# Performance work log

Hardware: AMD Instinct MI355X
Metric: run time of the kernel (lower is better)

The kernel has to match this reference:

```python
import jax, jax.numpy as jnp
import numpy as np

B, N = 2, 2000
C_IN, RH, RW = 256, 7, 7
D_FLAT = C_IN * RH * RW  # 12544
D_OUT = 1024
NUM_CLASSES = 10


def setup_inputs() -> dict:
    key = jax.random.key(0)
    ks = jax.random.split(key, 10)
    s1 = 1.0 / np.sqrt(D_FLAT)
    s2 = 1.0 / np.sqrt(D_OUT)
    return {
        "features": jax.random.normal(ks[0], (B, N, C_IN, RH, RW), jnp.float32),
        "boxes": jax.random.normal(ks[1], (B, N, 5), jnp.float32),
        "w1": jax.random.uniform(ks[2], (D_FLAT, D_OUT), jnp.float32, -s1, s1),
        "b1": jax.random.uniform(ks[3], (D_OUT,), jnp.float32, -s1, s1),
        "w2": jax.random.uniform(ks[4], (D_OUT, D_OUT), jnp.float32, -s2, s2),
        "b2": jax.random.uniform(ks[5], (D_OUT,), jnp.float32, -s2, s2),
        "wc": jax.random.uniform(ks[6], (D_OUT, NUM_CLASSES + 1), jnp.float32, -s2, s2),
        "bc": jax.random.uniform(ks[7], (NUM_CLASSES + 1,), jnp.float32, -s2, s2),
        "wr": jax.random.uniform(ks[8], (D_OUT, 5), jnp.float32, -s2, s2),
        "br": jax.random.uniform(ks[9], (5,), jnp.float32, -s2, s2),
    }


def reference(features, boxes, w1, b1, w2, b2, wc, bc, wr, br):
    # Flatten(start_dim=2): [B, N, C*7*7]
    x = features.reshape(B, N, D_FLAT)
    # fc: Linear -> ReLU -> Linear -> ReLU
    h = jax.nn.relu(jnp.einsum("bnd,de->bne", x, w1) + b1)
    h = jax.nn.relu(jnp.einsum("bnd,de->bne", h, w2) + b2)
    classification = jnp.einsum("bnd,dc->bnc", h, wc) + bc  # [B, N, num_classes+1]
    regression = jnp.einsum("bnd,dr->bnr", h, wr) + br      # [B, N, 5]
    boxes_out = boxes + regression
    rois = boxes
    return classification, boxes_out, rois
```

## Files before the change

kernel.cpp:

```cpp
#include <hip/hip_runtime.h>
#include <stdint.h>

#define GAS __attribute__((address_space(1)))
#define LAS __attribute__((address_space(3)))

typedef short bf16x8 __attribute__((ext_vector_type(8)));
typedef float f32x4 __attribute__((ext_vector_type(4)));
typedef unsigned short u16x8 __attribute__((ext_vector_type(8)));

__device__ __forceinline__ unsigned short f2bf(float f) {
  union { float f; uint32_t u; } v; v.f = f;
  uint32_t r = v.u + 0x7FFFu + ((v.u >> 16) & 1u);
  return (unsigned short)(r >> 16);
}

__global__ __launch_bounds__(256) void prep_transpose(const float* __restrict__ w1,
                                                      const float* __restrict__ w2,
                                                      unsigned short* __restrict__ W1T,
                                                      unsigned short* __restrict__ W2T) {
  __shared__ unsigned short tile[32][33];
  int tx = threadIdx.x, ty = threadIdx.y;
  const float* src;
  unsigned short* dst;
  int R, yb;
  if ((int)blockIdx.y < 392) {
    src = w1; dst = W1T; R = 12544; yb = blockIdx.y;
  } else {
    src = w2; dst = W2T; R = 1024; yb = blockIdx.y - 392;
  }
  const int C = 1024;
  int r0 = yb * 32, c0 = blockIdx.x * 32;
#pragma unroll
  for (int i = 0; i < 32; i += 8)
    tile[ty + i][tx] = f2bf(src[(long)(r0 + ty + i) * C + c0 + tx]);
  __syncthreads();
#pragma unroll
  for (int i = 0; i < 32; i += 8)
    dst[(long)(c0 + ty + i) * R + r0 + tx] = tile[tx][ty + i];
}

__global__ __launch_bounds__(256, 2) void gemm1_f32a(const float* __restrict__ A,
                                                     const unsigned short* __restrict__ Bt,
                                                     float* __restrict__ Cv, int M, int K,
                                                     int kIters) {
  __shared__ unsigned short lA[128 * 64];
  __shared__ unsigned short lB[128 * 64];
  const int tid = threadIdx.x;
  const int lane = tid & 63;
  const int wave = tid >> 6;
  const int wm = wave >> 1, wn = wave & 1;

  const int b = blockIdx.x;
  const int xcd = b & 7;
  const int slot = b >> 3;
  const int bx = slot & 7;
  const int pg = xcd * 16 + (slot >> 3);
  const int by = pg & 31;
  const int bz = pg >> 5;

  const long rowBase = (long)by * 128;
  const long colBase = (long)bx * 128;
  const int kStart = bz * kIters * 64;

  f32x4 acc[4][4];
#pragma unroll
  for (int i = 0; i < 4; i++)
#pragma unroll
    for (int j = 0; j < 4; j++) acc[i][j] = (f32x4){0.f, 0.f, 0.f, 0.f};

  long gA[4], gB[4];
  int aLds[4];
#pragma unroll
  for (int it = 0; it < 4; ++it) {
    int f = it * 256 + tid;
    int r = f >> 3;
    int q = f & 7;
    int kq = ((q ^ (r & 7)) * 8) + kStart;
    long ar = rowBase + r;
    if (ar >= M) ar = M - 1;
    gA[it] = ar * (long)K + kq;
    gB[it] = ((long)(colBase + r)) * K + kq;
    aLds[it] = f * 8;
  }

  for (int ki = 0; ki < kIters; ++ki) {
    const long kc = (long)ki * 64;
#pragma unroll
    for (int it = 0; it < 4; ++it) {
      int f = it * 256 + tid;
      __builtin_amdgcn_global_load_lds((const GAS void*)(Bt + gB[it] + kc),
                                       (LAS void*)(lB + f * 8), 16, 0, 0);
    }
#pragma unroll
    for (int it = 0; it < 4; ++it) {
      const float4* p = (const float4*)(A + gA[it] + kc);
      float4 a = p[0], c = p[1];
      u16x8 v;
      v[0] = f2bf(a.x); v[1] = f2bf(a.y); v[2] = f2bf(a.z); v[3] = f2bf(a.w);
      v[4] = f2bf(c.x); v[5] = f2bf(c.y); v[6] = f2bf(c.z); v[7] = f2bf(c.w);
      *(u16x8*)(lA + aLds[it]) = v;
    }
    __syncthreads();
#pragma unroll
    for (int ks = 0; ks < 64; ks += 32) {
      bf16x8 af[4], bf[4];
      const int c = (ks >> 3) + (lane >> 4);
      const int slotk = (c ^ (lane & 7)) << 3;
      const int mr = wm * 64 + (lane & 15);
      const int nr = wn * 64 + (lane & 15);
#pragma unroll
      for (int i = 0; i < 4; i++)
        af[i] = *(const bf16x8*)(lA + (mr + i * 16) * 64 + slotk);
#pragma unroll
      for (int i = 0; i < 4; i++)
        bf[i] = *(const bf16x8*)(lB + (nr + i * 16) * 64 + slotk);
#pragma unroll
      for (int i = 0; i < 4; i++)
#pragma unroll
        for (int j = 0; j < 4; j++)
          acc[i][j] = __builtin_amdgcn_mfma_f32_16x16x32_bf16(af[i], bf[j], acc[i][j], 0, 0, 0);
    }
    __syncthreads();
  }

  const int cq = lane & 15;
  const int rq = (lane >> 4) * 4;
#pragma unroll
  for (int i = 0; i < 4; i++) {
#pragma unroll
    for (int j = 0; j < 4; j++) {
      int col = (int)colBase + wn * 64 + j * 16 + cq;
#pragma unroll
      for (int r = 0; r < 4; r++) {
        long grow = rowBase + wm * 64 + i * 16 + rq + r;
        if (grow < M) unsafeAtomicAdd(&Cv[grow * 1024 + col], acc[i][j][r]);
      }
    }
  }
}

__global__ __launch_bounds__(256, 2) void gemm2_fused(const float* __restrict__ H1f,
                                                      const float* __restrict__ bias1,
                                                      const unsigned short* __restrict__ Bt,
                                                      const float* __restrict__ bias2,
                                                      float* __restrict__ Cv, int M) {
  const int K = 1024;
  __shared__ unsigned short lA[128 * 64];
  __shared__ unsigned short lB[64 * 64];
  const int tid = threadIdx.x;
  const int lane = tid & 63;
  const int wave = tid >> 6;
  const int wm = wave >> 1, wn = wave & 1;

  const int b = blockIdx.x;
  const int xcd = b & 7;
  const int slot = b >> 3;
  const int bx = slot & 15;
  const int by = xcd * 4 + (slot >> 4);

  const long rowBase = (long)by * 128;
  const long colBase = (long)bx * 64;

  f32x4 acc[4][2];
#pragma unroll
  for (int i = 0; i < 4; i++)
#pragma unroll
    for (int j = 0; j < 2; j++) acc[i][j] = (f32x4){0.f, 0.f, 0.f, 0.f};

  long gA[4];
  int aLds[4], aKq[4];
#pragma unroll
  for (int it = 0; it < 4; ++it) {
    int f = it * 256 + tid;
    int r = f >> 3;
    int q = f & 7;
    int kq = (q ^ (r & 7)) * 8;
    long ar = rowBase + r;
    if (ar >= M) ar = M - 1;
    gA[it] = ar * (long)K + kq;
    aLds[it] = f * 8;
    aKq[it] = kq;
  }
  long gB[2];
#pragma unroll
  for (int it = 0; it < 2; ++it) {
    int f = it * 256 + tid;
    int r = f >> 3;
    int q = f & 7;
    int kq = (q ^ (r & 7)) * 8;
    gB[it] = ((long)(colBase + r)) * K + kq;
  }

  for (int ki = 0; ki < 16; ++ki) {
    const long kc = (long)ki * 64;
#pragma unroll
    for (int it = 0; it < 2; ++it) {
      int f = it * 256 + tid;
      __builtin_amdgcn_global_load_lds((const GAS void*)(Bt + gB[it] + kc),
                                       (LAS void*)(lB + f * 8), 16, 0, 0);
    }
#pragma unroll
    for (int it = 0; it < 4; ++it) {
      const float4* p = (const float4*)(H1f + gA[it] + kc);
      const float4* bp = (const float4*)(bias1 + kc + aKq[it]);
      float4 a = p[0], c = p[1];
      float4 ba = bp[0], bb = bp[1];
      u16x8 v;
      v[0] = f2bf(fmaxf(a.x + ba.x, 0.f)); v[1] = f2bf(fmaxf(a.y + ba.y, 0.f));
      v[2] = f2bf(fmaxf(a.z + ba.z, 0.f)); v[3] = f2bf(fmaxf(a.w + ba.w, 0.f));
      v[4] = f2bf(fmaxf(c.x + bb.x, 0.f)); v[5] = f2bf(fmaxf(c.y + bb.y, 0.f));
      v[6] = f2bf(fmaxf(c.z + bb.z, 0.f)); v[7] = f2bf(fmaxf(c.w + bb.w, 0.f));
      *(u16x8*)(lA + aLds[it]) = v;
    }
    __syncthreads();
#pragma unroll
    for (int ks = 0; ks < 64; ks += 32) {
      bf16x8 af[4], bf[2];
      const int c = (ks >> 3) + (lane >> 4);
      const int slotk = (c ^ (lane & 7)) << 3;
      const int mr = wm * 64 + (lane & 15);
      const int nr = wn * 32 + (lane & 15);
#pragma unroll
      for (int i = 0; i < 4; i++)
        af[i] = *(const bf16x8*)(lA + (mr + i * 16) * 64 + slotk);
#pragma unroll
      for (int j = 0; j < 2; j++)
        bf[j] = *(const bf16x8*)(lB + (nr + j * 16) * 64 + slotk);
#pragma unroll
      for (int i = 0; i < 4; i++)
#pragma unroll
        for (int j = 0; j < 2; j++)
          acc[i][j] = __builtin_amdgcn_mfma_f32_16x16x32_bf16(af[i], bf[j], acc[i][j], 0, 0, 0);
    }
    __syncthreads();
  }

  const int cq = lane & 15;
  const int rq = (lane >> 4) * 4;
#pragma unroll
  for (int i = 0; i < 4; i++) {
#pragma unroll
    for (int j = 0; j < 2; j++) {
      int col = (int)colBase + wn * 32 + j * 16 + cq;
      float bv = bias2[col];
#pragma unroll
      for (int r = 0; r < 4; r++) {
        long grow = rowBase + wm * 64 + i * 16 + rq + r;
        if (grow < M) {
          float v = acc[i][j][r] + bv;
          Cv[grow * 1024 + col] = v > 0.f ? v : 0.f;
        }
      }
    }
  }
}

__global__ __launch_bounds__(256) void head_kernel(
    const float* __restrict__ H2, const float* __restrict__ wc, const float* __restrict__ bc,
    const float* __restrict__ wr, const float* __restrict__ br, const float* __restrict__ boxes,
    float* __restrict__ cls, float* __restrict__ bout, float* __restrict__ rois) {
  const int lane = threadIdx.x & 63;
  const int wave = threadIdx.x >> 6;
  const int row = blockIdx.x * 4 + wave;
  const float* h = H2 + (long)row * 1024;
  float acc[16];
#pragma unroll
  for (int c = 0; c < 16; c++) acc[c] = 0.f;
#pragma unroll
  for (int i = 0; i < 16; i++) {
    int d = i * 64 + lane;
    float hv = h[d];
#pragma unroll
    for (int c = 0; c < 11; c++) acc[c] += hv * wc[d * 11 + c];
#pragma unroll
    for (int c = 0; c < 5; c++) acc[11 + c] += hv * wr[d * 5 + c];
  }
#pragma unroll
  for (int off = 32; off >= 1; off >>= 1) {
#pragma unroll
    for (int c = 0; c < 16; c++) acc[c] += __shfl_down(acc[c], off);
  }
  if (lane == 0) {
#pragma unroll
    for (int c = 0; c < 11; c++) cls[row * 11 + c] = acc[c] + bc[c];
#pragma unroll
    for (int c = 0; c < 5; c++) {
      float rg = acc[11 + c] + br[c];
      float bx = boxes[row * 5 + c];
      bout[row * 5 + c] = bx + rg;
      rois[row * 5 + c] = bx;
    }
  }
}

extern "C" void kernel_launch(void* const* d_in, const int* in_sizes, int n_in,
                              void* d_out, int out_size, void* d_ws, size_t ws_size,
                              hipStream_t stream) {
  const float* features = (const float*)d_in[0];
  const float* boxes = (const float*)d_in[1];
  const float* w1 = (const float*)d_in[2];
  const float* b1 = (const float*)d_in[3];
  const float* w2 = (const float*)d_in[4];
  const float* b2 = (const float*)d_in[5];
  const float* wc = (const float*)d_in[6];
  const float* bc = (const float*)d_in[7];
  const float* wr = (const float*)d_in[8];
  const float* br = (const float*)d_in[9];

  char* ws = (char*)d_ws;
  unsigned short* W1T = (unsigned short*)ws;
  unsigned short* W2T = (unsigned short*)(ws + 25690112);
  float*          H1f = (float*)(ws + 27787264);
  float*          H2  = (float*)(ws + 44171264);

  hipMemsetAsync(H1f, 0, 16384000, stream);
  prep_transpose<<<dim3(32, 424), dim3(32, 8), 0, stream>>>(w1, w2, W1T, W2T);
  gemm1_f32a<<<1024, 256, 0, stream>>>(features, W1T, H1f, 4000, 12544, 49);
  gemm2_fused<<<512, 256, 0, stream>>>(H1f, b1, W2T, b2, H2, 4000);
  float* cls = (float*)d_out;
  float* bout = cls + 44000;
  float* rois = cls + 64000;
  head_kernel<<<1000, 256, 0, stream>>>(H2, wc, bc, wr, br, boxes, cls, bout, rois);
}
```

Measured before the change: 550.4 us.

## Pre-convert features to bf16 and load A via direct-to-LDS; transpose head weights

Adds a separate kernel that converts the fp32 feature matrix to bf16 once, so the first GEMM can stream A tiles with global_load_lds instead of loading fp32 through registers and converting per tile. The head weights are also transposed into a 16x1024 fp32 layout so the head kernel reads them with coalesced float4 loads. The cost is an extra pass that reads 200MB of fp32 features and writes 100MB of bf16, plus a larger workspace.

```diff
diff --git a/kernel.cpp b/kernel.cpp
--- a/kernel.cpp
+++ b/kernel.cpp
@@ -14,12 +14,38 @@
   return (unsigned short)(r >> 16);
 }
 
+__global__ __launch_bounds__(256) void cvt_kernel(const float* __restrict__ src,
+                                                  unsigned short* __restrict__ dst,
+                                                  long n8) {
+  long i = (long)blockIdx.x * blockDim.x + threadIdx.x;
+  if (i >= n8) return;
+  const float4* s4 = (const float4*)src;
+  float4 a = s4[i * 2];
+  float4 b = s4[i * 2 + 1];
+  u16x8 o;
+  o[0] = f2bf(a.x); o[1] = f2bf(a.y); o[2] = f2bf(a.z); o[3] = f2bf(a.w);
+  o[4] = f2bf(b.x); o[5] = f2bf(b.y); o[6] = f2bf(b.z); o[7] = f2bf(b.w);
+  ((u16x8*)dst)[i] = o;
+}
+
 __global__ __launch_bounds__(256) void prep_transpose(const float* __restrict__ w1,
                                                       const float* __restrict__ w2,
+                                                      const float* __restrict__ wc,
+                                                      const float* __restrict__ wr,
                                                       unsigned short* __restrict__ W1T,
-                                                      unsigned short* __restrict__ W2T) {
+                                                      unsigned short* __restrict__ W2T,
+                                                      float* __restrict__ WhT) {
+  int tx = threadIdx.x, ty = threadIdx.y;
+  if ((int)blockIdx.y == 424) {
+    int d = blockIdx.x * 32 + tx;
+#pragma unroll
+    for (int c = ty; c < 16; c += 8) {
+      float v = (c < 11) ? wc[d * 11 + c] : wr[d * 5 + (c - 11)];
+      WhT[c * 1024 + d] = v;
+    }
+    return;
+  }
   __shared__ unsigned short tile[32][33];
-  int tx = threadIdx.x, ty = threadIdx.y;
   const float* src;
   unsigned short* dst;
   int R, yb;
@@ -39,10 +65,10 @@
     dst[(long)(c0 + ty + i) * R + r0 + tx] = tile[tx][ty + i];
 }
 
-__global__ __launch_bounds__(256, 2) void gemm1_f32a(const float* __restrict__ A,
-                                                     const unsigned short* __restrict__ Bt,
-                                                     float* __restrict__ Cv, int M, int K,
-                                                     int kIters) {
+__global__ __launch_bounds__(256, 2) void gemm1_atomic(const unsigned short* __restrict__ A,
+                                                       const unsigned short* __restrict__ Bt,
+                                                       float* __restrict__ Cv, int M, int K,
+                                                       int kIters) {
   __shared__ unsigned short lA[128 * 64];
   __shared__ unsigned short lB[128 * 64];
   const int tid = threadIdx.x;
@@ -69,7 +95,6 @@
     for (int j = 0; j < 4; j++) acc[i][j] = (f32x4){0.f, 0.f, 0.f, 0.f};
 
   long gA[4], gB[4];
-  int aLds[4];
 #pragma unroll
   for (int it = 0; it < 4; ++it) {
     int f = it * 256 + tid;
@@ -80,25 +105,21 @@
     if (ar >= M) ar = M - 1;
     gA[it] = ar * (long)K + kq;
     gB[it] = ((long)(colBase + r)) * K + kq;
-    aLds[it] = f * 8;
   }
 
   for (int ki = 0; ki < kIters; ++ki) {
     const long kc = (long)ki * 64;
+#pragma unroll
+    for (int it = 0; it < 4; ++it) {
+      int f = it * 256 + tid;
+      __builtin_amdgcn_global_load_lds((const GAS void*)(A + gA[it] + kc),
+                                       (LAS void*)(lA + f * 8), 16, 0, 0);
+    }
 #pragma unroll
     for (int it = 0; it < 4; ++it) {
       int f = it * 256 + tid;
       __builtin_amdgcn_global_load_lds((const GAS void*)(Bt + gB[it] + kc),
                                        (LAS void*)(lB + f * 8), 16, 0, 0);
-    }
-#pragma unroll
-    for (int it = 0; it < 4; ++it) {
-      const float4* p = (const float4*)(A + gA[it] + kc);
-      float4 a = p[0], c = p[1];
-      u16x8 v;
-      v[0] = f2bf(a.x); v[1] = f2bf(a.y); v[2] = f2bf(a.z); v[3] = f2bf(a.w);
-      v[4] = f2bf(c.x); v[5] = f2bf(c.y); v[6] = f2bf(c.z); v[7] = f2bf(c.w);
-      *(u16x8*)(lA + aLds[it]) = v;
     }
     __syncthreads();
 #pragma unroll
@@ -255,25 +276,25 @@
   }
 }
 
-__global__ __launch_bounds__(256) void head_kernel(
-    const float* __restrict__ H2, const float* __restrict__ wc, const float* __restrict__ bc,
-    const float* __restrict__ wr, const float* __restrict__ br, const float* __restrict__ boxes,
+__global__ __launch_bounds__(256) void head_t(
+    const float* __restrict__ H2, const float* __restrict__ WhT, const float* __restrict__ bc,
+    const float* __restrict__ br, const float* __restrict__ boxes,
     float* __restrict__ cls, float* __restrict__ bout, float* __restrict__ rois) {
   const int lane = threadIdx.x & 63;
   const int wave = threadIdx.x >> 6;
   const int row = blockIdx.x * 4 + wave;
-  const float* h = H2 + (long)row * 1024;
+  const float4* h4 = (const float4*)(H2 + (long)row * 1024);
   float acc[16];
 #pragma unroll
   for (int c = 0; c < 16; c++) acc[c] = 0.f;
 #pragma unroll
-  for (int i = 0; i < 16; i++) {
-    int d = i * 64 + lane;
-    float hv = h[d];
-#pragma unroll
-    for (int c = 0; c < 11; c++) acc[c] += hv * wc[d * 11 + c];
-#pragma unroll
-    for (int c = 0; c < 5; c++) acc[11 + c] += hv * wr[d * 5 + c];
+  for (int i = 0; i < 4; i++) {
+    float4 hv = h4[i * 64 + lane];
+#pragma unroll
+    for (int c = 0; c < 16; c++) {
+      float4 wv = ((const float4*)(WhT + c * 1024))[i * 64 + lane];
+      acc[c] += hv.x * wv.x + hv.y * wv.y + hv.z * wv.z + hv.w * wv.w;
+    }
   }
 #pragma unroll
   for (int off = 32; off >= 1; off >>= 1) {
@@ -308,17 +329,20 @@
   const float* br = (const float*)d_in[9];
 
   char* ws = (char*)d_ws;
-  unsigned short* W1T = (unsigned short*)ws;
-  unsigned short* W2T = (unsigned short*)(ws + 25690112);
-  float*          H1f = (float*)(ws + 27787264);
-  float*          H2  = (float*)(ws + 44171264);
+  unsigned short* Xb  = (unsigned short*)ws;
+  unsigned short* W1T = (unsigned short*)(ws + 100352000);
+  unsigned short* W2T = (unsigned short*)(ws + 126042112);
+  float*          WhT = (float*)(ws + 128139264);
+  float*          H1f = (float*)(ws + 128204800);
+  float*          H2  = (float*)(ws + 144588800);
 
   hipMemsetAsync(H1f, 0, 16384000, stream);
-  prep_transpose<<<dim3(32, 424), dim3(32, 8), 0, stream>>>(w1, w2, W1T, W2T);
-  gemm1_f32a<<<1024, 256, 0, stream>>>(features, W1T, H1f, 4000, 12544, 49);
+  cvt_kernel<<<24500, 256, 0, stream>>>(features, Xb, 6272000);
+  prep_transpose<<<dim3(32, 425), dim3(32, 8), 0, stream>>>(w1, w2, wc, wr, W1T, W2T, WhT);
+  gemm1_atomic<<<1024, 256, 0, stream>>>(Xb, W1T, H1f, 4000, 12544, 49);
   gemm2_fused<<<512, 256, 0, stream>>>(H1f, b1, W2T, b2, H2, 4000);
   float* cls = (float*)d_out;
   float* bout = cls + 44000;
   float* rois = cls + 64000;
-  head_kernel<<<1000, 256, 0, stream>>>(H2, wc, bc, wr, br, boxes, cls, bout, rois);
-}
+  head_t<<<1000, 256, 0, stream>>>(H2, WhT, bc, br, boxes, cls, bout, rois);
+}
```

Result: faster. 532.4 us (-3.3%).
